# Optimization experiments

Hardware: AMD Instinct MI355X
Metric: run time of the kernel (lower is better)

The kernel has to match this reference:

```python
import jax, jax.numpy as jnp
import numpy as np

N_NODES = 20000
N_EDGES = 320000
HEADS = 4
N_REL = 40
F_IN = 768
HID = 128
N_CLS = 9


def setup_inputs() -> dict:
    key = jax.random.key(0)
    ks = jax.random.split(key, 32)
    s = 0.05
    inp = {
        'x': jax.random.normal(ks[0], (N_NODES, F_IN), jnp.float32),
        'edge_index': jax.random.randint(ks[1], (2, N_EDGES), 0, N_NODES, jnp.int64),
        'edge_type': jax.random.randint(ks[2], (N_EDGES,), 0, N_REL, jnp.int64),
        'edge_distance': jax.random.randint(ks[3], (N_EDGES,), 0, 10, jnp.int32),
        'W0': jax.random.normal(ks[4], (HEADS, F_IN, HID), jnp.float32) * s,
        'asrc0': jax.random.normal(ks[5], (HEADS, HID), jnp.float32) * s,
        'adst0': jax.random.normal(ks[6], (HEADS, HID), jnp.float32) * s,
        'aedge0': jax.random.normal(ks[7], (HEADS, 2), jnp.float32) * s,
        'b0': jnp.zeros((HID,), jnp.float32),
        'rel0': jax.random.normal(ks[8], (N_REL, 2), jnp.float32) * s,
        'Wm': jax.random.normal(ks[9], (3, HEADS, HID, HID), jnp.float32) * s,
        'asrcm': jax.random.normal(ks[10], (3, HEADS, HID), jnp.float32) * s,
        'adstm': jax.random.normal(ks[11], (3, HEADS, HID), jnp.float32) * s,
        'aedgem': jax.random.normal(ks[12], (3, HEADS, 2), jnp.float32) * s,
        'bm': jnp.zeros((3, HID), jnp.float32),
        'relm': jax.random.normal(ks[13], (3, N_REL, 2), jnp.float32) * s,
        'WL': jax.random.normal(ks[14], (HEADS, HID, N_CLS), jnp.float32) * s,
        'asrcL': jax.random.normal(ks[15], (HEADS, N_CLS), jnp.float32) * s,
        'adstL': jax.random.normal(ks[16], (HEADS, N_CLS), jnp.float32) * s,
        'aedgeL': jax.random.normal(ks[17], (HEADS, 2), jnp.float32) * s,
        'bL': jnp.zeros((N_CLS,), jnp.float32),
        'relL': jax.random.normal(ks[18], (N_REL, 2), jnp.float32) * s,
        'bn_gamma': jnp.ones((4, HID), jnp.float32),
        'bn_beta': jnp.zeros((4, HID), jnp.float32),
    }
    return inp


def _bn(x, g, b):
    # BatchNorm1d with batch statistics (training mode), eps=1e-5
    mu = x.mean(0)
    var = ((x - mu) ** 2).mean(0)
    return (x - mu) * jax.lax.rsqrt(var + 1e-5) * g + b


def _argcn_conv(x, src, dst, etype, distw, W, a_s, a_d, a_e, b, rel, n):
    # multi-head relational graph attention conv with distance decay
    h = jnp.einsum('nf,hfo->nho', x, W)                       # [N,H,O]
    es = jnp.einsum('nho,ho->nh', h, a_s)                     # [N,H]
    ed = jnp.einsum('nho,ho->nh', h, a_d)                     # [N,H]
    ee = rel[etype] @ a_e.T                                   # [E,H]
    logit = jax.nn.leaky_relu(es[src] + ed[dst] + ee, 0.2)    # [E,H]
    m = jax.ops.segment_max(logit, dst, num_segments=n)
    ex = jnp.exp(logit - m[dst])
    den = jax.ops.segment_sum(ex, dst, num_segments=n)
    alpha = ex / (den[dst] + 1e-16) * distw[:, None]          # [E,H]
    out = jax.ops.segment_sum(alpha[:, :, None] * h[src], dst, num_segments=n)  # [N,H,O]
    return out.mean(axis=1) + b


def reference(x, edge_index, edge_type, edge_distance,
              W0, asrc0, adst0, aedge0, b0, rel0,
              Wm, asrcm, adstm, aedgem, bm, relm,
              WL, asrcL, adstL, aedgeL, bL, relL,
              bn_gamma, bn_beta):
    n = x.shape[0]
    src, dst = edge_index[0], edge_index[1]
    distw = 1.0 / (1.0 + edge_distance.astype(jnp.float32))
    x = _argcn_conv(x, src, dst, edge_type, distw, W0, asrc0, adst0, aedge0, b0, rel0, n)
    for i in range(3):
        h = jax.nn.leaky_relu(_bn(x, bn_gamma[i], bn_beta[i]), 0.1)
        x = _argcn_conv(h, src, dst, edge_type, distw, Wm[i], asrcm[i], adstm[i], aedgem[i], bm[i], relm[i], n) + h
    h = jax.nn.leaky_relu(_bn(x, bn_gamma[3], bn_beta[3]), 0.1)
    x = _argcn_conv(h, src, dst, edge_type, distw, WL, asrcL, adstL, aedgeL, bL, relL, n)
    return jax.nn.leaky_relu(x, 0.1)
```

## Files before the change

### kernel.cpp

```cpp
#include <hip/hip_runtime.h>
#include <math.h>

#define NN   20000
#define NE   320000
#define NH   4
#define NREL 40
#define FIN  768
#define HIDD 128
#define NCLS 9
#define MAXDEG 128

typedef __attribute__((ext_vector_type(8))) short short8;
typedef __attribute__((ext_vector_type(4))) float f32x4;
typedef unsigned short b16;

__device__ __forceinline__ float lrelu(float v, float s) { return v > 0.f ? v : v * s; }
__device__ __forceinline__ b16 f2b(float f) {
    unsigned int u = __float_as_uint(f);
    unsigned int r = u + 0x7FFFu + ((u >> 16) & 1u);
    return (b16)(r >> 16);
}
__device__ __forceinline__ float b2f(b16 u) { return __uint_as_float(((unsigned int)u) << 16); }

__global__ void k_zero(float* p, int n) {
    int i = blockIdx.x * blockDim.x + threadIdx.x;
    if (i < n) p[i] = 0.f;
}
__global__ void k_copy_i32(int* d, const int* s, int n) {
    int i = blockIdx.x * blockDim.x + threadIdx.x;
    if (i < n) d[i] = s[i];
}

__global__ void k_count(const int* __restrict__ dst, int* __restrict__ counts) {
    int e = blockIdx.x * blockDim.x + threadIdx.x;
    if (e < NE) atomicAdd(&counts[dst[e]], 1);
}
__global__ void k_scan(const int* __restrict__ counts, int* __restrict__ rowptr) {
    __shared__ int sh[1024];
    int t = threadIdx.x;
    int base = t * 20;
    int sum = 0;
    if (t < 1000) for (int k = 0; k < 20; ++k) sum += counts[base + k];
    sh[t] = sum;
    __syncthreads();
    for (int off = 1; off < 1024; off <<= 1) {
        int v = (t >= off) ? sh[t - off] : 0;
        __syncthreads();
        sh[t] += v;
        __syncthreads();
    }
    int ex = (t == 0) ? 0 : sh[t - 1];
    if (t == 0) rowptr[0] = 0;
    if (t < 1000) {
        int run = ex;
        for (int k = 0; k < 20; ++k) {
            run += counts[base + k];
            rowptr[base + k + 1] = run;
        }
    }
}
__global__ void k_fill(const int* __restrict__ dst, int* __restrict__ cursor, int* __restrict__ eidx) {
    int e = blockIdx.x * blockDim.x + threadIdx.x;
    if (e < NE) {
        int pos = atomicAdd(&cursor[dst[e]], 1);
        eidx[pos] = e;
    }
}
__global__ void k_permute(const int* __restrict__ eidx, const int* __restrict__ src,
                          const int* __restrict__ etype, const int* __restrict__ dist,
                          int* __restrict__ srcp, int* __restrict__ etp,
                          float* __restrict__ distwp) {
    int p = blockIdx.x * blockDim.x + threadIdx.x;
    if (p >= NE) return;
    int e = eidx[p];
    srcp[p] = src[e];
    etp[p] = etype[e];
    distwp[p] = 1.f / (1.f + (float)dist[e]);
}

__global__ void k_etab(const float* __restrict__ rel0, const float* __restrict__ relm,
                       const float* __restrict__ relL, const float* __restrict__ ae0,
                       const float* __restrict__ aem, const float* __restrict__ aeL,
                       float* __restrict__ etab) {
    int id = blockIdx.x * blockDim.x + threadIdx.x;
    if (id >= 5 * NREL * NH) return;
    int tab = id / (NREL * NH);
    int rem = id % (NREL * NH);
    int t = rem >> 2, h = rem & 3;
    const float *rel, *ae;
    if (tab == 0)      { rel = rel0;                        ae = ae0; }
    else if (tab <= 3) { rel = relm + (tab - 1) * NREL * 2; ae = aem + (tab - 1) * NH * 2; }
    else               { rel = relL;                        ae = aeL; }
    etab[id] = rel[t * 2] * ae[h * 2] + rel[t * 2 + 1] * ae[h * 2 + 1];
}
__global__ void k_wsm(const float* __restrict__ Wm, const float* __restrict__ asrcm,
                      const float* __restrict__ adstm, float* __restrict__ wsm,
                      float* __restrict__ wdm) {
    int id = blockIdx.x * blockDim.x + threadIdx.x;
    if (id >= 2 * 3 * NH * HIDD) return;
    int which = id / (3 * NH * HIDD);
    int r = id % (3 * NH * HIDD);
    int ih = r / HIDD;
    int f = r % HIDD;
    const float* w = Wm + ((size_t)ih * HIDD + f) * HIDD;
    const float* a = (which ? adstm : asrcm) + ih * HIDD;
    float acc = 0.f;
    for (int o = 0; o < HIDD; ++o) acc += w[o] * a[o];
    (which ? wdm : wsm)[r] = acc;
}

__global__ void k_cast_bf16(const float* __restrict__ in, b16* __restrict__ out, int n4) {
    int i = blockIdx.x * blockDim.x + threadIdx.x;
    if (i >= n4) return;
    float4 v = ((const float4*)in)[i];
    ushort4 o;
    o.x = f2b(v.x); o.y = f2b(v.y); o.z = f2b(v.z); o.w = f2b(v.w);
    ((ushort4*)out)[i] = o;
}
__global__ void k_convB0(const float* __restrict__ W0, b16* __restrict__ B0t) {
    int id = blockIdx.x * blockDim.x + threadIdx.x;
    if (id >= 512 * FIN) return;
    int c = id / FIN, k = id % FIN;
    int h = c >> 7, o = c & 127;
    B0t[id] = f2b(W0[((size_t)h * FIN + k) * HIDD + o]);
}
__global__ void k_convBm(const float* __restrict__ Wm, b16* __restrict__ Bmt) {
    int id = blockIdx.x * blockDim.x + threadIdx.x;
    if (id >= 3 * HIDD * 512) return;
    int i = id / (HIDD * 512);
    int r = id % (HIDD * 512);
    int o = r / 512, hf = r % 512;
    Bmt[id] = f2b(Wm[(size_t)i * 512 * HIDD + (size_t)hf * HIDD + o]);
}
__global__ void k_convBL(const float* __restrict__ WL, b16* __restrict__ WLt) {
    int id = blockIdx.x * blockDim.x + threadIdx.x;
    if (id >= 48 * HIDD) return;
    int cf = id / HIDD, k = id % HIDD;
    float v = 0.f;
    if (cf < 36) {
        int h = cf / 9, c = cf % 9;
        v = WL[((size_t)h * HIDD + k) * NCLS + c];
    }
    WLt[id] = f2b(v);
}

__global__ __launch_bounds__(256) void k_mfma_gemm(
    const b16* __restrict__ A, const b16* __restrict__ Bt, int M, int K, int N,
    float scl, b16* __restrict__ Cb, float* __restrict__ Cf,
    const float* __restrict__ bias, const float* __restrict__ resid,
    const float* __restrict__ asv, const float* __restrict__ adv,
    float* __restrict__ esp, float* __restrict__ edp) {
    __shared__ b16 As[128][40];
    __shared__ b16 Bs[128][40];
    __shared__ float sc_es[2][128];
    __shared__ float sc_ed[2][128];
    int tid = threadIdx.x;
    int lane = tid & 63, wave = tid >> 6;
    int wm = wave >> 1, wn = wave & 1;
    int l16 = lane & 15, quad = lane >> 4;
    int row0 = blockIdx.x * 128, col0 = blockIdx.y * 128;

    int c0 = tid, c1 = tid + 256;
    int ar0 = c0 >> 2, as0 = (c0 & 3) << 3;
    int ar1 = c1 >> 2, as1 = (c1 & 3) << 3;
    bool va0 = (row0 + ar0) < M, va1 = (row0 + ar1) < M;
    const b16* Ap0 = A + (size_t)(row0 + ar0) * K + as0;
    const b16* Ap1 = A + (size_t)(row0 + ar1) * K + as1;
    const b16* Bp0 = Bt + (size_t)(col0 + ar0) * K + as0;
    const b16* Bp1 = Bt + (size_t)(col0 + ar1) * K + as1;

    f32x4 acc[4][4];
#pragma unroll
    for (int i = 0; i < 4; ++i)
#pragma unroll
        for (int j = 0; j < 4; ++j) acc[i][j] = (f32x4){0.f, 0.f, 0.f, 0.f};
    short8 zz = {0, 0, 0, 0, 0, 0, 0, 0};

    for (int kt = 0; kt < K; kt += 32) {
        short8 a0 = va0 ? *(const short8*)(Ap0 + kt) : zz;
        short8 a1 = va1 ? *(const short8*)(Ap1 + kt) : zz;
        short8 b0 = *(const short8*)(Bp0 + kt);
        short8 b1 = *(const short8*)(Bp1 + kt);
        __syncthreads();
        *(short8*)&As[ar0][as0] = a0;
        *(short8*)&As[ar1][as1] = a1;
        *(short8*)&Bs[ar0][as0] = b0;
        *(short8*)&Bs[ar1][as1] = b1;
        __syncthreads();
        short8 bf[4];
#pragma unroll
        for (int ni = 0; ni < 4; ++ni)
            bf[ni] = *(const short8*)&Bs[wn * 64 + ni * 16 + l16][quad * 8];
#pragma unroll
        for (int mi = 0; mi < 4; ++mi) {
            short8 af = *(const short8*)&As[wm * 64 + mi * 16 + l16][quad * 8];
#pragma unroll
            for (int ni = 0; ni < 4; ++ni)
                acc[mi][ni] = __builtin_amdgcn_mfma_f32_16x16x32_bf16(af, bf[ni], acc[mi][ni], 0, 0, 0);
        }
    }
    if (Cb) {
#pragma unroll
        for (int mi = 0; mi < 4; ++mi) {
            int rb = row0 + wm * 64 + mi * 16 + quad * 4;
#pragma unroll
            for (int ni = 0; ni < 4; ++ni) {
                int c = col0 + wn * 64 + ni * 16 + l16;
#pragma unroll
                for (int r = 0; r < 4; ++r) {
                    int row = rb + r;
                    if (row < M) Cb[(size_t)row * N + c] = f2b(acc[mi][ni][r]);
                }
            }
        }
    } else {
#pragma unroll
        for (int mi = 0; mi < 4; ++mi) {
            int rb = row0 + wm * 64 + mi * 16 + quad * 4;
#pragma unroll
            for (int ni = 0; ni < 4; ++ni) {
                int c = col0 + wn * 64 + ni * 16 + l16;
#pragma unroll
                for (int r = 0; r < 4; ++r) {
                    int row = rb + r;
                    if (row < M) {
                        float v = acc[mi][ni][r] * scl + bias[c] + resid[(size_t)row * N + c];
                        Cf[(size_t)row * N + c] = v;
                    }
                }
            }
        }
    }
    if (esp) {
        int h = blockIdx.y;
        float as_c[4], ad_c[4];
#pragma unroll
        for (int ni = 0; ni < 4; ++ni) {
            int c = wn * 64 + ni * 16 + l16;
            as_c[ni] = asv[h * 128 + c];
            ad_c[ni] = adv[h * 128 + c];
        }
#pragma unroll
        for (int mi = 0; mi < 4; ++mi) {
#pragma unroll
            for (int r = 0; r < 4; ++r) {
                float pes = 0.f, ped = 0.f;
#pragma unroll
                for (int ni = 0; ni < 4; ++ni) {
                    float v = acc[mi][ni][r];
                    pes += v * as_c[ni];
                    ped += v * ad_c[ni];
                }
#pragma unroll
                for (int m = 1; m < 16; m <<= 1) {
                    pes += __shfl_xor(pes, m, 64);
                    ped += __shfl_xor(ped, m, 64);
                }
                if (l16 == 0) {
                    int rl = wm * 64 + mi * 16 + quad * 4 + r;
                    sc_es[wn][rl] = pes;
                    sc_ed[wn][rl] = ped;
                }
            }
        }
        __syncthreads();
        if (tid < 128) {
            int row = row0 + tid;
            if (row < M) {
                esp[row * 4 + h] = sc_es[0][tid] + sc_es[1][tid];
                edp[row * 4 + h] = sc_ed[0][tid] + sc_ed[1][tid];
            }
        }
    }
}

__global__ __launch_bounds__(256) void k_gemmL_mfma(
    const b16* __restrict__ hbb, const b16* __restrict__ WLt, float* __restrict__ hL) {
    int tid = threadIdx.x;
    int lane = tid & 63, wave = tid >> 6;
    int l16 = lane & 15, quad = lane >> 4;
    int base = blockIdx.x * 64 + wave * 16;
    int na = base + l16;
    f32x4 acc[3];
#pragma unroll
    for (int ct = 0; ct < 3; ++ct) acc[ct] = (f32x4){0.f, 0.f, 0.f, 0.f};
    short8 zz = {0, 0, 0, 0, 0, 0, 0, 0};
#pragma unroll
    for (int k0 = 0; k0 < 128; k0 += 32) {
        short8 af = (na < NN) ? *(const short8*)(hbb + (size_t)na * HIDD + k0 + quad * 8) : zz;
#pragma unroll
        for (int ct = 0; ct < 3; ++ct) {
            short8 bf = *(const short8*)(WLt + (size_t)(ct * 16 + l16) * HIDD + k0 + quad * 8);
            acc[ct] = __builtin_amdgcn_mfma_f32_16x16x32_bf16(af, bf, acc[ct], 0, 0, 0);
        }
    }
#pragma unroll
    for (int ct = 0; ct < 3; ++ct) {
        int col = ct * 16 + l16;
        if (col < 36) {
#pragma unroll
            for (int r = 0; r < 4; ++r) {
                int row = base + quad * 4 + r;
                if (row < NN) hL[(size_t)row * 36 + col] = acc[ct][r];
            }
        }
    }
}

__global__ void k_scoresL(const float* __restrict__ hL, const float* __restrict__ aS,
                          const float* __restrict__ aD, float* __restrict__ es,
                          float* __restrict__ ed) {
    int n = blockIdx.x * blockDim.x + threadIdx.x;
    if (n >= NN) return;
    for (int h = 0; h < NH; ++h) {
        float s = 0.f, d = 0.f;
        for (int c = 0; c < NCLS; ++c) {
            float v = hL[(size_t)n * 36 + h * 9 + c];
            s += v * aS[h * 9 + c];
            d += v * aD[h * 9 + c];
        }
        es[n * 4 + h] = s;
        ed[n * 4 + h] = d;
    }
}

__global__ __launch_bounds__(64) void k_agg0_f(
    const int* __restrict__ rowptr, const int* __restrict__ srcp,
    const int* __restrict__ etpp, const float* __restrict__ distwp,
    const float* __restrict__ es, const float* __restrict__ ed,
    const float* __restrict__ etab, const b16* __restrict__ h0b,
    const float* __restrict__ b0, float* __restrict__ xout) {
    __shared__ float4 exw[MAXDEG];
    int n = blockIdx.x, t = threadIdx.x;
    int p0 = rowptr[n], p1 = rowptr[n + 1];
    int deg = p1 - p0;
    float4 edn = ((const float4*)ed)[n];
    float d0 = 0.f, d1 = 0.f, d2 = 0.f, d3 = 0.f;
    for (int p = p0 + t; p < p1; p += 64) {
        int s = srcp[p], ty = etpp[p];
        float w = distwp[p];
        float4 a = ((const float4*)es)[s];
        float4 c = ((const float4*)etab)[ty];
        float e0 = __expf(lrelu(a.x + edn.x + c.x, 0.2f));
        float e1 = __expf(lrelu(a.y + edn.y + c.y, 0.2f));
        float e2 = __expf(lrelu(a.z + edn.z + c.z, 0.2f));
        float e3 = __expf(lrelu(a.w + edn.w + c.w, 0.2f));
        d0 += e0; d1 += e1; d2 += e2; d3 += e3;
        int ix = p - p0;
        if (ix < MAXDEG) exw[ix] = make_float4(e0 * w, e1 * w, e2 * w, e3 * w);
    }
#pragma unroll
    for (int off = 32; off > 0; off >>= 1) {
        d0 += __shfl_down(d0, off, 64);
        d1 += __shfl_down(d1, off, 64);
        d2 += __shfl_down(d2, off, 64);
        d3 += __shfl_down(d3, off, 64);
    }
    d0 = __shfl(d0, 0, 64); d1 = __shfl(d1, 0, 64);
    d2 = __shfl(d2, 0, 64); d3 = __shfl(d3, 0, 64);
    float r0 = 1.f / (d0 + 1e-16f), r1 = 1.f / (d1 + 1e-16f);
    float r2 = 1.f / (d2 + 1e-16f), r3 = 1.f / (d3 + 1e-16f);
    __syncthreads();
    float acc0 = 0.f, acc1 = 0.f;
    int tt = t * 2;
    if (deg <= MAXDEG) {
        int p = p0;
        for (; p + 4 <= p1; p += 4) {
            int ib = p - p0;
            int ss[4]; float4 ee[4];
#pragma unroll
            for (int j = 0; j < 4; ++j) { ss[j] = srcp[p + j]; ee[j] = exw[ib + j]; }
#pragma unroll
            for (int j = 0; j < 4; ++j) {
                const b16* hr = h0b + (size_t)ss[j] * 512;
                ushort2 u0 = *(const ushort2*)(hr + tt);
                ushort2 u1 = *(const ushort2*)(hr + 128 + tt);
                ushort2 u2 = *(const ushort2*)(hr + 256 + tt);
                ushort2 u3 = *(const ushort2*)(hr + 384 + tt);
                float c0 = ee[j].x * r0, c1 = ee[j].y * r1;
                float c2 = ee[j].z * r2, c3 = ee[j].w * r3;
                acc0 += c0 * b2f(u0.x) + c1 * b2f(u1.x) + c2 * b2f(u2.x) + c3 * b2f(u3.x);
                acc1 += c0 * b2f(u0.y) + c1 * b2f(u1.y) + c2 * b2f(u2.y) + c3 * b2f(u3.y);
            }
        }
        for (; p < p1; ++p) {
            int s = srcp[p];
            float4 e = exw[p - p0];
            const b16* hr = h0b + (size_t)s * 512;
            ushort2 u0 = *(const ushort2*)(hr + tt);
            ushort2 u1 = *(const ushort2*)(hr + 128 + tt);
            ushort2 u2 = *(const ushort2*)(hr + 256 + tt);
            ushort2 u3 = *(const ushort2*)(hr + 384 + tt);
            float c0 = e.x * r0, c1 = e.y * r1, c2 = e.z * r2, c3 = e.w * r3;
            acc0 += c0 * b2f(u0.x) + c1 * b2f(u1.x) + c2 * b2f(u2.x) + c3 * b2f(u3.x);
            acc1 += c0 * b2f(u0.y) + c1 * b2f(u1.y) + c2 * b2f(u2.y) + c3 * b2f(u3.y);
        }
    } else {
        for (int p = p0; p < p1; ++p) {
            int s = srcp[p];
            int ix = p - p0;
            float4 e;
            if (ix < MAXDEG) e = exw[ix];
            else {
                int ty = etpp[p];
                float w = distwp[p];
                float4 a = ((const float4*)es)[s];
                float4 c = ((const float4*)etab)[ty];
                e.x = __expf(lrelu(a.x + edn.x + c.x, 0.2f)) * w;
                e.y = __expf(lrelu(a.y + edn.y + c.y, 0.2f)) * w;
                e.z = __expf(lrelu(a.z + edn.z + c.z, 0.2f)) * w;
                e.w = __expf(lrelu(a.w + edn.w + c.w, 0.2f)) * w;
            }
            const b16* hr = h0b + (size_t)s * 512;
            ushort2 u0 = *(const ushort2*)(hr + tt);
            ushort2 u1 = *(const ushort2*)(hr + 128 + tt);
            ushort2 u2 = *(const ushort2*)(hr + 256 + tt);
            ushort2 u3 = *(const ushort2*)(hr + 384 + tt);
            float c0 = e.x * r0, c1 = e.y * r1, c2 = e.z * r2, c3 = e.w * r3;
            acc0 += c0 * b2f(u0.x) + c1 * b2f(u1.x) + c2 * b2f(u2.x) + c3 * b2f(u3.x);
            acc1 += c0 * b2f(u0.y) + c1 * b2f(u1.y) + c2 * b2f(u2.y) + c3 * b2f(u3.y);
        }
    }
    xout[(size_t)n * HIDD + tt] = 0.25f * acc0 + b0[tt];
    xout[(size_t)n * HIDD + tt + 1] = 0.25f * acc1 + b0[tt + 1];
}
__global__ __launch_bounds__(64) void k_aggmid_f(
    const int* __restrict__ rowptr, const int* __restrict__ srcp,
    const int* __restrict__ etpp, const float* __restrict__ distwp,
    const float* __restrict__ es, const float* __restrict__ ed,
    const float* __restrict__ etab, const b16* __restrict__ hbb,
    b16* __restrict__ aggb) {
    __shared__ float4 exw[MAXDEG];
    int n = blockIdx.x, t = threadIdx.x;
    int p0 = rowptr[n], p1 = rowptr[n + 1];
    int deg = p1 - p0;
    float4 edn = ((const float4*)ed)[n];
    float d0 = 0.f, d1 = 0.f, d2 = 0.f, d3 = 0.f;
    for (int p = p0 + t; p < p1; p += 64) {
        int s = srcp[p], ty = etpp[p];
        float w = distwp[p];
        float4 a = ((const float4*)es)[s];
        float4 c = ((const float4*)etab)[ty];
        float e0 = __expf(lrelu(a.x + edn.x + c.x, 0.2f));
        float e1 = __expf(lrelu(a.y + edn.y + c.y, 0.2f));
        float e2 = __expf(lrelu(a.z + edn.z + c.z, 0.2f));
        float e3 = __expf(lrelu(a.w + edn.w + c.w, 0.2f));
        d0 += e0; d1 += e1; d2 += e2; d3 += e3;
        int ix = p - p0;
        if (ix < MAXDEG) exw[ix] = make_float4(e0 * w, e1 * w, e2 * w, e3 * w);
    }
#pragma unroll
    for (int off = 32; off > 0; off >>= 1) {
        d0 += __shfl_down(d0, off, 64);
        d1 += __shfl_down(d1, off, 64);
        d2 += __shfl_down(d2, off, 64);
        d3 += __shfl_down(d3, off, 64);
    }
    d0 = __shfl(d0, 0, 64); d1 = __shfl(d1, 0, 64);
    d2 = __shfl(d2, 0, 64); d3 = __shfl(d3, 0, 64);
    float r0 = 1.f / (d0 + 1e-16f), r1 = 1.f / (d1 + 1e-16f);
    float r2 = 1.f / (d2 + 1e-16f), r3 = 1.f / (d3 + 1e-16f);
    __syncthreads();
    float a00 = 0.f, a01 = 0.f, a10 = 0.f, a11 = 0.f;
    float a20 = 0.f, a21 = 0.f, a30 = 0.f, a31 = 0.f;
    int tt = t * 2;
    if (deg <= MAXDEG) {
        int p = p0;
        for (; p + 4 <= p1; p += 4) {
            int ib = p - p0;
            int ss[4]; float4 ee[4];
#pragma unroll
            for (int j = 0; j < 4; ++j) { ss[j] = srcp[p + j]; ee[j] = exw[ib + j]; }
#pragma unroll
            for (int j = 0; j < 4; ++j) {
                ushort2 u = *(const ushort2*)(hbb + (size_t)ss[j] * HIDD + tt);
                float f0 = b2f(u.x), f1 = b2f(u.y);
                float c0 = ee[j].x * r0, c1 = ee[j].y * r1;
                float c2 = ee[j].z * r2, c3 = ee[j].w * r3;
                a00 += c0 * f0; a01 += c0 * f1;
                a10 += c1 * f0; a11 += c1 * f1;
                a20 += c2 * f0; a21 += c2 * f1;
                a30 += c3 * f0; a31 += c3 * f1;
            }
        }
        for (; p < p1; ++p) {
            int s = srcp[p];
            float4 e = exw[p - p0];
            ushort2 u = *(const ushort2*)(hbb + (size_t)s * HIDD + tt);
            float f0 = b2f(u.x), f1 = b2f(u.y);
            float c0 = e.x * r0, c1 = e.y * r1, c2 = e.z * r2, c3 = e.w * r3;
            a00 += c0 * f0; a01 += c0 * f1;
            a10 += c1 * f0; a11 += c1 * f1;
            a20 += c2 * f0; a21 += c2 * f1;
            a30 += c3 * f0; a31 += c3 * f1;
        }
    } else {
        for (int p = p0; p < p1; ++p) {
            int s = srcp[p];
            int ix = p - p0;
            float4 e;
            if (ix < MAXDEG) e = exw[ix];
            else {
                int ty = etpp[p];
                float w = distwp[p];
                float4 a = ((const float4*)es)[s];
                float4 c = ((const float4*)etab)[ty];
                e.x = __expf(lrelu(a.x + edn.x + c.x, 0.2f)) * w;
                e.y = __expf(lrelu(a.y + edn.y + c.y, 0.2f)) * w;
                e.z = __expf(lrelu(a.z + edn.z + c.z, 0.2f)) * w;
                e.w = __expf(lrelu(a.w + edn.w + c.w, 0.2f)) * w;
            }
            ushort2 u = *(const ushort2*)(hbb + (size_t)s * HIDD + tt);
            float f0 = b2f(u.x), f1 = b2f(u.y);
            float c0 = e.x * r0, c1 = e.y * r1, c2 = e.z * r2, c3 = e.w * r3;
            a00 += c0 * f0; a01 += c0 * f1;
            a10 += c1 * f0; a11 += c1 * f1;
            a20 += c2 * f0; a21 += c2 * f1;
            a30 += c3 * f0; a31 += c3 * f1;
        }
    }
    b16* o = aggb + (size_t)n * 512;
    ushort2 w0; w0.x = f2b(a00); w0.y = f2b(a01); *(ushort2*)(o + tt) = w0;
    ushort2 w1; w1.x = f2b(a10); w1.y = f2b(a11); *(ushort2*)(o + 128 + tt) = w1;
    ushort2 w2; w2.x = f2b(a20); w2.y = f2b(a21); *(ushort2*)(o + 256 + tt) = w2;
    ushort2 w3; w3.x = f2b(a30); w3.y = f2b(a31); *(ushort2*)(o + 384 + tt) = w3;
}
__global__ __launch_bounds__(64) void k_aggL_f(
    const int* __restrict__ rowptr, const int* __restrict__ srcp,
    const int* __restrict__ etpp, const float* __restrict__ distwp,
    const float* __restrict__ es, const float* __restrict__ ed,
    const float* __restrict__ etab, const float* __restrict__ hL,
    const float* __restrict__ bL, float* __restrict__ out) {
    __shared__ float4 exw[MAXDEG];
    __shared__ float sh[40];
    int n = blockIdx.x, t = threadIdx.x;
    int p0 = rowptr[n], p1 = rowptr[n + 1];
    float4 edn = ((const float4*)ed)[n];
    float d0 = 0.f, d1 = 0.f, d2 = 0.f, d3 = 0.f;
    for (int p = p0 + t; p < p1; p += 64) {
        int s = srcp[p], ty = etpp[p];
        float w = distwp[p];
        float4 a = ((const float4*)es)[s];
        float4 c = ((const float4*)etab)[ty];
        float e0 = __expf(lrelu(a.x + edn.x + c.x, 0.2f));
        float e1 = __expf(lrelu(a.y + edn.y + c.y, 0.2f));
        float e2 = __expf(lrelu(a.z + edn.z + c.z, 0.2f));
        float e3 = __expf(lrelu(a.w + edn.w + c.w, 0.2f));
        d0 += e0; d1 += e1; d2 += e2; d3 += e3;
        int ix = p - p0;
        if (ix < MAXDEG) exw[ix] = make_float4(e0 * w, e1 * w, e2 * w, e3 * w);
    }
#pragma unroll
    for (int off = 32; off > 0; off >>= 1) {
        d0 += __shfl_down(d0, off, 64);
        d1 += __shfl_down(d1, off, 64);
        d2 += __shfl_down(d2, off, 64);
        d3 += __shfl_down(d3, off, 64);
    }
    d0 = __shfl(d0, 0, 64); d1 = __shfl(d1, 0, 64);
    d2 = __shfl(d2, 0, 64); d3 = __shfl(d3, 0, 64);
    __syncthreads();
    if (t < 36) {
        int hh = t / 9;
        float rv = (hh == 0) ? 1.f / (d0 + 1e-16f)
                 : (hh == 1) ? 1.f / (d1 + 1e-16f)
                 : (hh == 2) ? 1.f / (d2 + 1e-16f)
                             : 1.f / (d3 + 1e-16f);
        float acc = 0.f;
        for (int p = p0; p < p1; ++p) {
            int s = srcp[p];
            int ix = p - p0;
            float av;
            if (ix < MAXDEG) {
                float4 e = exw[ix];
                av = (hh == 0) ? e.x : (hh == 1) ? e.y : (hh == 2) ? e.z : e.w;
            } else {
                int ty = etpp[p];
                float w = distwp[p];
                float a4 = ((const float4*)es)[s].x;
                float4 a = ((const float4*)es)[s];
                float4 c = ((const float4*)etab)[ty];
                float lv = (hh == 0) ? a.x + edn.x + c.x
                         : (hh == 1) ? a.y + edn.y + c.y
                         : (hh == 2) ? a.z + edn.z + c.z
                                     : a.w + edn.w + c.w;
                av = __expf(lrelu(lv, 0.2f)) * w;
                (void)a4;
            }
            acc += av * rv * hL[(size_t)s * 36 + t];
        }
        sh[t] = acc;
    }
    __syncthreads();
    if (t < 9) {
        float v = 0.25f * (sh[t] + sh[t + 9] + sh[t + 18] + sh[t + 27]) + bL[t];
        out[(size_t)n * 9 + t] = lrelu(v, 0.1f);
    }
}

__global__ __launch_bounds__(128) void k_bnstats(const float* __restrict__ x, float* __restrict__ partial) {
    int f = threadIdx.x;
    float s = 0.f, q = 0.f;
    for (int r = blockIdx.x; r < NN; r += gridDim.x) {
        float v = x[(size_t)r * HIDD + f];
        s += v;
        q += v * v;
    }
    partial[blockIdx.x * 256 + f] = s;
    partial[blockIdx.x * 256 + 128 + f] = q;
}
__global__ void k_bnfinal(const float* __restrict__ partial, const float* __restrict__ gamma,
                          const float* __restrict__ beta, float* __restrict__ scale,
                          float* __restrict__ shift) {
    int f = threadIdx.x;
    float s = 0.f, q = 0.f;
    for (int j = 0; j < 200; ++j) {
        s += partial[j * 256 + f];
        q += partial[j * 256 + 128 + f];
    }
    float m = s * (1.f / NN);
    float v = q * (1.f / NN) - m * m;
    float sc = gamma[f] * rsqrtf(v + 1e-5f);
    scale[f] = sc;
    shift[f] = beta[f] - m * sc;
}
__global__ __launch_bounds__(64) void k_bnaps(
    const float* __restrict__ x, const float* __restrict__ scale,
    const float* __restrict__ shift, const float* __restrict__ Ws,
    const float* __restrict__ Wd, float* __restrict__ hb, b16* __restrict__ hbb,
    float* __restrict__ es, float* __restrict__ ed) {
    int n = blockIdx.x, t = threadIdx.x;
    float2 xv = ((const float2*)(x + (size_t)n * HIDD))[t];
    float2 sc = ((const float2*)scale)[t];
    float2 sh = ((const float2*)shift)[t];
    float y0 = lrelu(xv.x * sc.x + sh.x, 0.1f);
    float y1 = lrelu(xv.y * sc.y + sh.y, 0.1f);
    ((float2*)(hb + (size_t)n * HIDD))[t] = make_float2(y0, y1);
    ushort2 ub; ub.x = f2b(y0); ub.y = f2b(y1);
    ((ushort2*)(hbb + (size_t)n * HIDD))[t] = ub;
    if (Ws) {
        float pe[4], pd[4];
        int tt = t * 2;
#pragma unroll
        for (int h = 0; h < 4; ++h) {
            pe[h] = y0 * Ws[h * 128 + tt] + y1 * Ws[h * 128 + tt + 1];
            pd[h] = y0 * Wd[h * 128 + tt] + y1 * Wd[h * 128 + tt + 1];
        }
#pragma unroll
        for (int off = 32; off > 0; off >>= 1) {
#pragma unroll
            for (int h = 0; h < 4; ++h) {
                pe[h] += __shfl_down(pe[h], off, 64);
                pd[h] += __shfl_down(pd[h], off, 64);
            }
        }
        if (t == 0) {
#pragma unroll
            for (int h = 0; h < 4; ++h) {
                es[n * 4 + h] = pe[h];
                ed[n * 4 + h] = pd[h];
            }
        }
    }
}

extern "C" void kernel_launch(void* const* d_in, const int* in_sizes, int n_in,
                              void* d_out, int out_size, void* d_ws, size_t ws_size,
                              hipStream_t stream) {
    const float* x = (const float*)d_in[0];
    const int* ei = (const int*)d_in[1];
    const int* src = ei;
    const int* dst = ei + NE;
    const int* etype = (const int*)d_in[2];
    const int* edist = (const int*)d_in[3];
    const float* W0 = (const float*)d_in[4];
    const float* asrc0 = (const float*)d_in[5];
    const float* adst0 = (const float*)d_in[6];
    const float* aedge0 = (const float*)d_in[7];
    const float* b0 = (const float*)d_in[8];
    const float* rel0 = (const float*)d_in[9];
    const float* Wm = (const float*)d_in[10];
    const float* asrcm = (const float*)d_in[11];
    const float* adstm = (const float*)d_in[12];
    const float* aedgem = (const float*)d_in[13];
    const float* bm = (const float*)d_in[14];
    const float* relm = (const float*)d_in[15];
    const float* WL = (const float*)d_in[16];
    const float* asrcL = (const float*)d_in[17];
    const float* adstL = (const float*)d_in[18];
    const float* aedgeL = (const float*)d_in[19];
    const float* bL = (const float*)d_in[20];
    const float* relL = (const float*)d_in[21];
    const float* bng = (const float*)d_in[22];
    const float* bnb = (const float*)d_in[23];
    float* out = (float*)d_out;

    char* w = (char*)d_ws;
    size_t off = 0;
    auto alloc = [&](size_t bytes) -> char* {
        char* p = w + off;
        off = (off + bytes + 255) & ~(size_t)255;
        return p;
    };
    char* ws0 = alloc((size_t)NN * FIN * 2);
    b16* xb = (b16*)ws0;
    float* xbuf = (float*)ws0;
    float* hb = (float*)(ws0 + 10240000);
    float* hL = (float*)(ws0 + 20480000);
    b16* h0b = (b16*)alloc((size_t)NN * 512 * 2);
    b16* B0t = (b16*)alloc((size_t)512 * FIN * 2);
    b16* Bmt = (b16*)alloc((size_t)3 * HIDD * 512 * 2);
    b16* WLt = (b16*)alloc((size_t)48 * HIDD * 2);
    b16* hbb = (b16*)alloc((size_t)NN * HIDD * 2);
    float* es = (float*)alloc((size_t)NN * 4 * 4);
    float* ed = (float*)alloc((size_t)NN * 4 * 4);
    int* srcp = (int*)alloc((size_t)NE * 4);
    int* etpp = (int*)alloc((size_t)NE * 4);
    float* distwp = (float*)alloc((size_t)NE * 4);
    int* eidx = (int*)alloc((size_t)NE * 4);
    float* bnpart = (float*)alloc((size_t)200 * 256 * 4);
    float* scale = (float*)alloc(128 * 4);
    float* shift = (float*)alloc(128 * 4);
    float* wsmb = (float*)alloc(1536 * 4);
    float* wdmb = (float*)alloc(1536 * 4);
    float* etab = (float*)alloc(800 * 4);
    int* counts = (int*)alloc((size_t)NN * 4);
    int* rowptr = (int*)alloc((size_t)(NN + 1) * 4);
    int* cursor = (int*)alloc((size_t)NN * 4);

    const int B256 = 256;
    int gNE = (NE + 255) / 256;
    int gNN = (NN + 255) / 256;

    k_zero<<<gNN, B256, 0, stream>>>((float*)counts, NN);
    k_count<<<gNE, B256, 0, stream>>>(dst, counts);
    k_scan<<<1, 1024, 0, stream>>>(counts, rowptr);
    k_copy_i32<<<gNN, B256, 0, stream>>>(cursor, rowptr, NN);
    k_fill<<<gNE, B256, 0, stream>>>(dst, cursor, eidx);
    k_permute<<<gNE, B256, 0, stream>>>(eidx, src, etype, edist, srcp, etpp, distwp);

    k_etab<<<4, B256, 0, stream>>>(rel0, relm, relL, aedge0, aedgem, aedgeL, etab);
    k_wsm<<<12, B256, 0, stream>>>(Wm, asrcm, adstm, wsmb, wdmb);
    k_cast_bf16<<<(NN * FIN / 4 + 255) / 256, B256, 0, stream>>>(x, xb, NN * FIN / 4);
    k_convB0<<<(512 * FIN + 255) / 256, B256, 0, stream>>>(W0, B0t);
    k_convBm<<<(3 * HIDD * 512 + 255) / 256, B256, 0, stream>>>(Wm, Bmt);
    k_convBL<<<(48 * HIDD + 255) / 256, B256, 0, stream>>>(WL, WLt);

    int mblk = (NN + 127) / 128;

    {
        dim3 g(mblk, 4);
        k_mfma_gemm<<<g, 256, 0, stream>>>(xb, B0t, NN, FIN, 512, 1.f, h0b, nullptr,
                                           nullptr, nullptr, asrc0, adst0, es, ed);
        k_agg0_f<<<NN, 64, 0, stream>>>(rowptr, srcp, etpp, distwp, es, ed, etab + 0,
                                        h0b, b0, xbuf);
    }

    for (int i = 0; i < 3; ++i) {
        k_bnstats<<<200, 128, 0, stream>>>(xbuf, bnpart);
        k_bnfinal<<<1, 128, 0, stream>>>(bnpart, bng + i * 128, bnb + i * 128, scale, shift);
        k_bnaps<<<NN, 64, 0, stream>>>(xbuf, scale, shift, wsmb + i * 512, wdmb + i * 512,
                                       hb, hbb, es, ed);
        k_aggmid_f<<<NN, 64, 0, stream>>>(rowptr, srcp, etpp, distwp, es, ed,
                                          etab + (1 + i) * 160, hbb, h0b);
        dim3 g(mblk, 1);
        k_mfma_gemm<<<g, 256, 0, stream>>>(h0b, Bmt + (size_t)i * HIDD * 512, NN, 512, HIDD,
                                           0.25f, nullptr, xbuf, bm + i * 128, hb,
                                           nullptr, nullptr, nullptr, nullptr);
    }

    {
        k_bnstats<<<200, 128, 0, stream>>>(xbuf, bnpart);
        k_bnfinal<<<1, 128, 0, stream>>>(bnpart, bng + 3 * 128, bnb + 3 * 128, scale, shift);
        k_bnaps<<<NN, 64, 0, stream>>>(xbuf, scale, shift, nullptr, nullptr, hb, hbb, es, ed);
        k_gemmL_mfma<<<(NN + 63) / 64, 256, 0, stream>>>(hbb, WLt, hL);
        k_scoresL<<<gNN, B256, 0, stream>>>(hL, asrcL, adstL, es, ed);
        k_aggL_f<<<NN, 64, 0, stream>>>(rowptr, srcp, etpp, distwp, es, ed, etab + 4 * 160,
                                        hL, bL, out);
    }
}
```

Measured before the change: 663.1 us.

## Fuse setup kernels, BN stats into GEMM epilogue, and scores into final GEMM

Several small preprocessing kernels are merged into two launches (tables and casts). BatchNorm statistics are accumulated by atomics inside the mid-layer GEMM epilogue, and normalization finalization moves into the apply kernel, which drops the separate stats and final kernels. The final-layer attention scores are computed in the GEMM epilogue, and the mid GEMM uses 64-row tiles for more blocks. Aggregation kernels are reorganized so each thread handles 4 contiguous channels over half the heads. Atomic float sums add nondeterminism, and the single-pass variance formula is kept.

```diff
diff --git a/kernel.cpp b/kernel.cpp
--- a/kernel.cpp
+++ b/kernel.cpp
@@ -22,9 +22,10 @@
 }
 __device__ __forceinline__ float b2f(b16 u) { return __uint_as_float(((unsigned int)u) << 16); }
 
-__global__ void k_zero(float* p, int n) {
+__global__ void k_init(int* __restrict__ counts, float* __restrict__ sums) {
     int i = blockIdx.x * blockDim.x + threadIdx.x;
-    if (i < n) p[i] = 0.f;
+    if (i < NN) counts[i] = 0;
+    if (i < 1024) sums[i] = 0.f;
 }
 __global__ void k_copy_i32(int* d, const int* s, int n) {
     int i = blockIdx.x * blockDim.x + threadIdx.x;
@@ -78,77 +79,82 @@
     distwp[p] = 1.f / (1.f + (float)dist[e]);
 }
 
-__global__ void k_etab(const float* __restrict__ rel0, const float* __restrict__ relm,
-                       const float* __restrict__ relL, const float* __restrict__ ae0,
-                       const float* __restrict__ aem, const float* __restrict__ aeL,
-                       float* __restrict__ etab) {
+__global__ void k_tables(const float* __restrict__ rel0, const float* __restrict__ relm,
+                         const float* __restrict__ relL, const float* __restrict__ ae0,
+                         const float* __restrict__ aem, const float* __restrict__ aeL,
+                         const float* __restrict__ Wm, const float* __restrict__ asrcm,
+                         const float* __restrict__ adstm, const float* __restrict__ WL,
+                         const float* __restrict__ asrcL, const float* __restrict__ adstL,
+                         float* __restrict__ etab, float* __restrict__ wsm,
+                         float* __restrict__ wdm, b16* __restrict__ WLt,
+                         float* __restrict__ aS48, float* __restrict__ aD48) {
     int id = blockIdx.x * blockDim.x + threadIdx.x;
-    if (id >= 5 * NREL * NH) return;
-    int tab = id / (NREL * NH);
-    int rem = id % (NREL * NH);
-    int t = rem >> 2, h = rem & 3;
-    const float *rel, *ae;
-    if (tab == 0)      { rel = rel0;                        ae = ae0; }
-    else if (tab <= 3) { rel = relm + (tab - 1) * NREL * 2; ae = aem + (tab - 1) * NH * 2; }
-    else               { rel = relL;                        ae = aeL; }
-    etab[id] = rel[t * 2] * ae[h * 2] + rel[t * 2 + 1] * ae[h * 2 + 1];
-}
-__global__ void k_wsm(const float* __restrict__ Wm, const float* __restrict__ asrcm,
-                      const float* __restrict__ adstm, float* __restrict__ wsm,
-                      float* __restrict__ wdm) {
+    if (id < 800) {
+        int tab = id / (NREL * NH);
+        int rem = id % (NREL * NH);
+        int t = rem >> 2, h = rem & 3;
+        const float *rel, *ae;
+        if (tab == 0)      { rel = rel0;                        ae = ae0; }
+        else if (tab <= 3) { rel = relm + (tab - 1) * NREL * 2; ae = aem + (tab - 1) * NH * 2; }
+        else               { rel = relL;                        ae = aeL; }
+        etab[id] = rel[t * 2] * ae[h * 2] + rel[t * 2 + 1] * ae[h * 2 + 1];
+    } else if (id < 3872) {
+        int id2 = id - 800;
+        int which = id2 / 1536;
+        int r = id2 % 1536;
+        int ih = r / HIDD;
+        int f = r % HIDD;
+        const float* w = Wm + ((size_t)ih * HIDD + f) * HIDD;
+        const float* a = (which ? adstm : asrcm) + ih * HIDD;
+        float acc = 0.f;
+        for (int o = 0; o < HIDD; ++o) acc += w[o] * a[o];
+        (which ? wdm : wsm)[r] = acc;
+    } else if (id < 10016) {
+        int id3 = id - 3872;
+        int cf = id3 / HIDD, k = id3 % HIDD;
+        float v = 0.f;
+        if (cf < 36) {
+            int h = cf / 9, c = cf % 9;
+            v = WL[((size_t)h * HIDD + k) * NCLS + c];
+        }
+        WLt[id3] = f2b(v);
+    } else if (id < 10112) {
+        int id4 = id - 10016;
+        int c = id4 % 48;
+        float v = (c < 36) ? ((id4 < 48) ? asrcL[c] : adstL[c]) : 0.f;
+        if (id4 < 48) aS48[c] = v; else aD48[c] = v;
+    }
+}
+
+#define XCAST4   3840000
+#define B0_END   4233216
+#define BM_END   4429824
+__global__ void k_casts(const float* __restrict__ x, const float* __restrict__ W0,
+                        const float* __restrict__ Wm, b16* __restrict__ xb,
+                        b16* __restrict__ B0t, b16* __restrict__ Bmt) {
     int id = blockIdx.x * blockDim.x + threadIdx.x;
-    if (id >= 2 * 3 * NH * HIDD) return;
-    int which = id / (3 * NH * HIDD);
-    int r = id % (3 * NH * HIDD);
-    int ih = r / HIDD;
-    int f = r % HIDD;
-    const float* w = Wm + ((size_t)ih * HIDD + f) * HIDD;
-    const float* a = (which ? adstm : asrcm) + ih * HIDD;
-    float acc = 0.f;
-    for (int o = 0; o < HIDD; ++o) acc += w[o] * a[o];
-    (which ? wdm : wsm)[r] = acc;
-}
-
-__global__ void k_cast_bf16(const float* __restrict__ in, b16* __restrict__ out, int n4) {
-    int i = blockIdx.x * blockDim.x + threadIdx.x;
-    if (i >= n4) return;
-    float4 v = ((const float4*)in)[i];
-    ushort4 o;
-    o.x = f2b(v.x); o.y = f2b(v.y); o.z = f2b(v.z); o.w = f2b(v.w);
-    ((ushort4*)out)[i] = o;
-}
-__global__ void k_convB0(const float* __restrict__ W0, b16* __restrict__ B0t) {
-    int id = blockIdx.x * blockDim.x + threadIdx.x;
-    if (id >= 512 * FIN) return;
-    int c = id / FIN, k = id % FIN;
-    int h = c >> 7, o = c & 127;
-    B0t[id] = f2b(W0[((size_t)h * FIN + k) * HIDD + o]);
-}
-__global__ void k_convBm(const float* __restrict__ Wm, b16* __restrict__ Bmt) {
-    int id = blockIdx.x * blockDim.x + threadIdx.x;
-    if (id >= 3 * HIDD * 512) return;
-    int i = id / (HIDD * 512);
-    int r = id % (HIDD * 512);
-    int o = r / 512, hf = r % 512;
-    Bmt[id] = f2b(Wm[(size_t)i * 512 * HIDD + (size_t)hf * HIDD + o]);
-}
-__global__ void k_convBL(const float* __restrict__ WL, b16* __restrict__ WLt) {
-    int id = blockIdx.x * blockDim.x + threadIdx.x;
-    if (id >= 48 * HIDD) return;
-    int cf = id / HIDD, k = id % HIDD;
-    float v = 0.f;
-    if (cf < 36) {
-        int h = cf / 9, c = cf % 9;
-        v = WL[((size_t)h * HIDD + k) * NCLS + c];
-    }
-    WLt[id] = f2b(v);
+    if (id < XCAST4) {
+        float4 v = ((const float4*)x)[id];
+        ushort4 o;
+        o.x = f2b(v.x); o.y = f2b(v.y); o.z = f2b(v.z); o.w = f2b(v.w);
+        ((ushort4*)xb)[id] = o;
+    } else if (id < B0_END) {
+        int i = id - XCAST4;
+        int c = i / FIN, k = i % FIN;
+        int h = c >> 7, o = c & 127;
+        B0t[i] = f2b(W0[((size_t)h * FIN + k) * HIDD + o]);
+    } else if (id < BM_END) {
+        int i = id - B0_END;
+        int l = i / (HIDD * 512);
+        int r = i % (HIDD * 512);
+        int o = r / 512, hf = r % 512;
+        Bmt[i] = f2b(Wm[(size_t)l * 512 * HIDD + (size_t)hf * HIDD + o]);
+    }
 }
 
 __global__ __launch_bounds__(256) void k_mfma_gemm(
     const b16* __restrict__ A, const b16* __restrict__ Bt, int M, int K, int N,
-    float scl, b16* __restrict__ Cb, float* __restrict__ Cf,
-    const float* __restrict__ bias, const float* __restrict__ resid,
-    const float* __restrict__ asv, const float* __restrict__ adv,
+    b16* __restrict__ Cb, const float* __restrict__ asv, const float* __restrict__ adv,
     float* __restrict__ esp, float* __restrict__ edp) {
     __shared__ b16 As[128][40];
     __shared__ b16 Bs[128][40];
@@ -199,39 +205,20 @@
                 acc[mi][ni] = __builtin_amdgcn_mfma_f32_16x16x32_bf16(af, bf[ni], acc[mi][ni], 0, 0, 0);
         }
     }
-    if (Cb) {
-#pragma unroll
-        for (int mi = 0; mi < 4; ++mi) {
-            int rb = row0 + wm * 64 + mi * 16 + quad * 4;
-#pragma unroll
-            for (int ni = 0; ni < 4; ++ni) {
-                int c = col0 + wn * 64 + ni * 16 + l16;
-#pragma unroll
-                for (int r = 0; r < 4; ++r) {
-                    int row = rb + r;
-                    if (row < M) Cb[(size_t)row * N + c] = f2b(acc[mi][ni][r]);
-                }
-            }
-        }
-    } else {
-#pragma unroll
-        for (int mi = 0; mi < 4; ++mi) {
-            int rb = row0 + wm * 64 + mi * 16 + quad * 4;
-#pragma unroll
-            for (int ni = 0; ni < 4; ++ni) {
-                int c = col0 + wn * 64 + ni * 16 + l16;
-#pragma unroll
-                for (int r = 0; r < 4; ++r) {
-                    int row = rb + r;
-                    if (row < M) {
-                        float v = acc[mi][ni][r] * scl + bias[c] + resid[(size_t)row * N + c];
-                        Cf[(size_t)row * N + c] = v;
-                    }
-                }
-            }
-        }
-    }
-    if (esp) {
+#pragma unroll
+    for (int mi = 0; mi < 4; ++mi) {
+        int rb = row0 + wm * 64 + mi * 16 + quad * 4;
+#pragma unroll
+        for (int ni = 0; ni < 4; ++ni) {
+            int c = col0 + wn * 64 + ni * 16 + l16;
+#pragma unroll
+            for (int r = 0; r < 4; ++r) {
+                int row = rb + r;
+                if (row < M) Cb[(size_t)row * N + c] = f2b(acc[mi][ni][r]);
+            }
+        }
+    }
+    {
         int h = blockIdx.y;
         float as_c[4], ad_c[4];
 #pragma unroll
@@ -274,8 +261,104 @@
     }
 }
 
+__global__ __launch_bounds__(128) void k_gemm_mid(
+    const b16* __restrict__ A, const b16* __restrict__ Bt, float* __restrict__ Cf,
+    const float* __restrict__ bias, const float* __restrict__ resid,
+    float* __restrict__ sums) {
+    __shared__ b16 As[64][40];
+    __shared__ b16 Bs[128][40];
+    int tid = threadIdx.x;
+    int lane = tid & 63, wave = tid >> 6;
+    int l16 = lane & 15, quad = lane >> 4;
+    int row0 = blockIdx.x * 64;
+    const int K = 512;
+
+    int ar[2], asg[2]; bool av[2];
+    const b16* Ap[2];
+#pragma unroll
+    for (int j = 0; j < 2; ++j) {
+        int c = tid + j * 128;
+        ar[j] = c >> 2; asg[j] = (c & 3) << 3;
+        int grow = row0 + ar[j];
+        av[j] = grow < NN;
+        Ap[j] = A + (size_t)(av[j] ? grow : 0) * K + asg[j];
+    }
+    int br[4], bsg[4];
+    const b16* Bp[4];
+#pragma unroll
+    for (int j = 0; j < 4; ++j) {
+        int c = tid + j * 128;
+        br[j] = c >> 2; bsg[j] = (c & 3) << 3;
+        Bp[j] = Bt + (size_t)br[j] * K + bsg[j];
+    }
+
+    f32x4 acc[4][4];
+#pragma unroll
+    for (int i = 0; i < 4; ++i)
+#pragma unroll
+        for (int j = 0; j < 4; ++j) acc[i][j] = (f32x4){0.f, 0.f, 0.f, 0.f};
+    short8 zz = {0, 0, 0, 0, 0, 0, 0, 0};
+
+    for (int kt = 0; kt < K; kt += 32) {
+        short8 a[2], b[4];
+#pragma unroll
+        for (int j = 0; j < 2; ++j) a[j] = av[j] ? *(const short8*)(Ap[j] + kt) : zz;
+#pragma unroll
+        for (int j = 0; j < 4; ++j) b[j] = *(const short8*)(Bp[j] + kt);
+        __syncthreads();
+#pragma unroll
+        for (int j = 0; j < 2; ++j) *(short8*)&As[ar[j]][asg[j]] = a[j];
+#pragma unroll
+        for (int j = 0; j < 4; ++j) *(short8*)&Bs[br[j]][bsg[j]] = b[j];
+        __syncthreads();
+        short8 bf[4];
+#pragma unroll
+        for (int ni = 0; ni < 4; ++ni)
+            bf[ni] = *(const short8*)&Bs[wave * 64 + ni * 16 + l16][quad * 8];
+#pragma unroll
+        for (int mi = 0; mi < 4; ++mi) {
+            short8 af = *(const short8*)&As[mi * 16 + l16][quad * 8];
+#pragma unroll
+            for (int ni = 0; ni < 4; ++ni)
+                acc[mi][ni] = __builtin_amdgcn_mfma_f32_16x16x32_bf16(af, bf[ni], acc[mi][ni], 0, 0, 0);
+        }
+    }
+    float sp[4] = {0.f, 0.f, 0.f, 0.f}, qp[4] = {0.f, 0.f, 0.f, 0.f};
+#pragma unroll
+    for (int mi = 0; mi < 4; ++mi) {
+        int rb = row0 + mi * 16 + quad * 4;
+#pragma unroll
+        for (int ni = 0; ni < 4; ++ni) {
+            int c = wave * 64 + ni * 16 + l16;
+#pragma unroll
+            for (int r = 0; r < 4; ++r) {
+                int row = rb + r;
+                if (row < NN) {
+                    float v = acc[mi][ni][r] * 0.25f + bias[c] + resid[(size_t)row * HIDD + c];
+                    Cf[(size_t)row * HIDD + c] = v;
+                    sp[ni] += v;
+                    qp[ni] += v * v;
+                }
+            }
+        }
+    }
+#pragma unroll
+    for (int ni = 0; ni < 4; ++ni) {
+        float s = sp[ni], q = qp[ni];
+        s += __shfl_xor(s, 16, 64); s += __shfl_xor(s, 32, 64);
+        q += __shfl_xor(q, 16, 64); q += __shfl_xor(q, 32, 64);
+        if (quad == 0) {
+            int c = wave * 64 + ni * 16 + l16;
+            atomicAdd(&sums[c], s);
+            atomicAdd(&sums[128 + c], q);
+        }
+    }
+}
+
 __global__ __launch_bounds__(256) void k_gemmL_mfma(
-    const b16* __restrict__ hbb, const b16* __restrict__ WLt, float* __restrict__ hL) {
+    const b16* __restrict__ hbb, const b16* __restrict__ WLt, float* __restrict__ hL,
+    const float* __restrict__ aS48, const float* __restrict__ aD48,
+    float* __restrict__ es, float* __restrict__ ed) {
     int tid = threadIdx.x;
     int lane = tid & 63, wave = tid >> 6;
     int l16 = lane & 15, quad = lane >> 4;
@@ -305,22 +388,45 @@
             }
         }
     }
-}
-
-__global__ void k_scoresL(const float* __restrict__ hL, const float* __restrict__ aS,
-                          const float* __restrict__ aD, float* __restrict__ es,
-                          float* __restrict__ ed) {
-    int n = blockIdx.x * blockDim.x + threadIdx.x;
-    if (n >= NN) return;
-    for (int h = 0; h < NH; ++h) {
-        float s = 0.f, d = 0.f;
-        for (int c = 0; c < NCLS; ++c) {
-            float v = hL[(size_t)n * 36 + h * 9 + c];
-            s += v * aS[h * 9 + c];
-            d += v * aD[h * 9 + c];
-        }
-        es[n * 4 + h] = s;
-        ed[n * 4 + h] = d;
+    float asv[3], adv[3]; int hh[3];
+#pragma unroll
+    for (int ct = 0; ct < 3; ++ct) {
+        int col = ct * 16 + l16;
+        asv[ct] = aS48[col];
+        adv[ct] = aD48[col];
+        hh[ct] = (col < 36) ? (col / 9) : 0;
+    }
+#pragma unroll
+    for (int r = 0; r < 4; ++r) {
+        float pes[4] = {0.f, 0.f, 0.f, 0.f}, ped[4] = {0.f, 0.f, 0.f, 0.f};
+#pragma unroll
+        for (int ct = 0; ct < 3; ++ct) {
+            float vs = acc[ct][r] * asv[ct];
+            float vd = acc[ct][r] * adv[ct];
+#pragma unroll
+            for (int h = 0; h < 4; ++h) {
+                pes[h] += (hh[ct] == h) ? vs : 0.f;
+                ped[h] += (hh[ct] == h) ? vd : 0.f;
+            }
+        }
+#pragma unroll
+        for (int m = 1; m < 16; m <<= 1) {
+#pragma unroll
+            for (int h = 0; h < 4; ++h) {
+                pes[h] += __shfl_xor(pes[h], m, 64);
+                ped[h] += __shfl_xor(ped[h], m, 64);
+            }
+        }
+        if (l16 == 0) {
+            int row = base + quad * 4 + r;
+            if (row < NN) {
+#pragma unroll
+                for (int h = 0; h < 4; ++h) {
+                    es[row * 4 + h] = pes[h];
+                    ed[row * 4 + h] = ped[h];
+                }
+            }
+        }
     }
 }
 
@@ -331,6 +437,7 @@
     const float* __restrict__ etab, const b16* __restrict__ h0b,
     const float* __restrict__ b0, float* __restrict__ xout) {
     __shared__ float4 exw[MAXDEG];
+    __shared__ float comb[32][4];
     int n = blockIdx.x, t = threadIdx.x;
     int p0 = rowptr[n], p1 = rowptr[n + 1];
     int deg = p1 - p0;
@@ -361,39 +468,42 @@
     float r0 = 1.f / (d0 + 1e-16f), r1 = 1.f / (d1 + 1e-16f);
     float r2 = 1.f / (d2 + 1e-16f), r3 = 1.f / (d3 + 1e-16f);
     __syncthreads();
-    float acc0 = 0.f, acc1 = 0.f;
-    int tt = t * 2;
+    int half = t >> 5, q = t & 31;
+    int cq = q * 4;
+    float ra = half ? r2 : r0, rb = half ? r3 : r1;
+    int sega = half * 256;
+    float acc[4] = {0.f, 0.f, 0.f, 0.f};
     if (deg <= MAXDEG) {
         int p = p0;
         for (; p + 4 <= p1; p += 4) {
-            int ib = p - p0;
             int ss[4]; float4 ee[4];
 #pragma unroll
-            for (int j = 0; j < 4; ++j) { ss[j] = srcp[p + j]; ee[j] = exw[ib + j]; }
+            for (int j = 0; j < 4; ++j) { ss[j] = srcp[p + j]; ee[j] = exw[p - p0 + j]; }
 #pragma unroll
             for (int j = 0; j < 4; ++j) {
-                const b16* hr = h0b + (size_t)ss[j] * 512;
-                ushort2 u0 = *(const ushort2*)(hr + tt);
-                ushort2 u1 = *(const ushort2*)(hr + 128 + tt);
-                ushort2 u2 = *(const ushort2*)(hr + 256 + tt);
-                ushort2 u3 = *(const ushort2*)(hr + 384 + tt);
-                float c0 = ee[j].x * r0, c1 = ee[j].y * r1;
-                float c2 = ee[j].z * r2, c3 = ee[j].w * r3;
-                acc0 += c0 * b2f(u0.x) + c1 * b2f(u1.x) + c2 * b2f(u2.x) + c3 * b2f(u3.x);
-                acc1 += c0 * b2f(u0.y) + c1 * b2f(u1.y) + c2 * b2f(u2.y) + c3 * b2f(u3.y);
+                float ca = (half ? ee[j].z : ee[j].x) * ra;
+                float cb = (half ? ee[j].w : ee[j].y) * rb;
+                const b16* hr = h0b + (size_t)ss[j] * 512 + sega + cq;
+                ushort4 ua = *(const ushort4*)(hr);
+                ushort4 ub = *(const ushort4*)(hr + 128);
+                acc[0] += ca * b2f(ua.x) + cb * b2f(ub.x);
+                acc[1] += ca * b2f(ua.y) + cb * b2f(ub.y);
+                acc[2] += ca * b2f(ua.z) + cb * b2f(ub.z);
+                acc[3] += ca * b2f(ua.w) + cb * b2f(ub.w);
             }
         }
         for (; p < p1; ++p) {
             int s = srcp[p];
             float4 e = exw[p - p0];
-            const b16* hr = h0b + (size_t)s * 512;
-            ushort2 u0 = *(const ushort2*)(hr + tt);
-            ushort2 u1 = *(const ushort2*)(hr + 128 + tt);
-            ushort2 u2 = *(const ushort2*)(hr + 256 + tt);
-            ushort2 u3 = *(const ushort2*)(hr + 384 + tt);
-            float c0 = e.x * r0, c1 = e.y * r1, c2 = e.z * r2, c3 = e.w * r3;
-            acc0 += c0 * b2f(u0.x) + c1 * b2f(u1.x) + c2 * b2f(u2.x) + c3 * b2f(u3.x);
-            acc1 += c0 * b2f(u0.y) + c1 * b2f(u1.y) + c2 * b2f(u2.y) + c3 * b2f(u3.y);
+            float ca = (half ? e.z : e.x) * ra;
+            float cb = (half ? e.w : e.y) * rb;
+            const b16* hr = h0b + (size_t)s * 512 + sega + cq;
+            ushort4 ua = *(const ushort4*)(hr);
+            ushort4 ub = *(const ushort4*)(hr + 128);
+            acc[0] += ca * b2f(ua.x) + cb * b2f(ub.x);
+            acc[1] += ca * b2f(ua.y) + cb * b2f(ub.y);
+            acc[2] += ca * b2f(ua.z) + cb * b2f(ub.z);
+            acc[3] += ca * b2f(ua.w) + cb * b2f(ub.w);
         }
     } else {
         for (int p = p0; p < p1; ++p) {
@@ -411,18 +521,30 @@
                 e.z = __expf(lrelu(a.z + edn.z + c.z, 0.2f)) * w;
                 e.w = __expf(lrelu(a.w + edn.w + c.w, 0.2f)) * w;
             }
-            const b16* hr = h0b + (size_t)s * 512;
-            ushort2 u0 = *(const ushort2*)(hr + tt);
-            ushort2 u1 = *(const ushort2*)(hr + 128 + tt);
-            ushort2 u2 = *(const ushort2*)(hr + 256 + tt);
-            ushort2 u3 = *(const ushort2*)(hr + 384 + tt);
-            float c0 = e.x * r0, c1 = e.y * r1, c2 = e.z * r2, c3 = e.w * r3;
-            acc0 += c0 * b2f(u0.x) + c1 * b2f(u1.x) + c2 * b2f(u2.x) + c3 * b2f(u3.x);
-            acc1 += c0 * b2f(u0.y) + c1 * b2f(u1.y) + c2 * b2f(u2.y) + c3 * b2f(u3.y);
-        }
-    }
-    xout[(size_t)n * HIDD + tt] = 0.25f * acc0 + b0[tt];
-    xout[(size_t)n * HIDD + tt + 1] = 0.25f * acc1 + b0[tt + 1];
+            float ca = (half ? e.z : e.x) * ra;
+            float cb = (half ? e.w : e.y) * rb;
+            const b16* hr = h0b + (size_t)s * 512 + sega + cq;
+            ushort4 ua = *(const ushort4*)(hr);
+            ushort4 ub = *(const ushort4*)(hr + 128);
+            acc[0] += ca * b2f(ua.x) + cb * b2f(ub.x);
+            acc[1] += ca * b2f(ua.y) + cb * b2f(ub.y);
+            acc[2] += ca * b2f(ua.z) + cb * b2f(ub.z);
+            acc[3] += ca * b2f(ua.w) + cb * b2f(ub.w);
+        }
+    }
+    if (half == 1) {
+        comb[q][0] = acc[0]; comb[q][1] = acc[1];
+        comb[q][2] = acc[2]; comb[q][3] = acc[3];
+    }
+    __syncthreads();
+    if (half == 0) {
+        float4 o;
+        o.x = 0.25f * (acc[0] + comb[q][0]) + b0[cq];
+        o.y = 0.25f * (acc[1] + comb[q][1]) + b0[cq + 1];
+        o.z = 0.25f * (acc[2] + comb[q][2]) + b0[cq + 2];
+        o.w = 0.25f * (acc[3] + comb[q][3]) + b0[cq + 3];
+        *(float4*)(xout + (size_t)n * HIDD + cq) = o;
+    }
 }
 __global__ __launch_bounds__(64) void k_aggmid_f(
     const int* __restrict__ rowptr, const int* __restrict__ srcp,
@@ -431,6 +553,7 @@
     const float* __restrict__ etab, const b16* __restrict__ hbb,
     b16* __restrict__ aggb) {
     __shared__ float4 exw[MAXDEG];
+    __shared__ float comb[32][16];
     int n = blockIdx.x, t = threadIdx.x;
     int p0 = rowptr[n], p1 = rowptr[n + 1];
     int deg = p1 - p0;
@@ -461,41 +584,33 @@
     float r0 = 1.f / (d0 + 1e-16f), r1 = 1.f / (d1 + 1e-16f);
     float r2 = 1.f / (d2 + 1e-16f), r3 = 1.f / (d3 + 1e-16f);
     __syncthreads();
-    float a00 = 0.f, a01 = 0.f, a10 = 0.f, a11 = 0.f;
-    float a20 = 0.f, a21 = 0.f, a30 = 0.f, a31 = 0.f;
-    int tt = t * 2;
+    int half = t >> 5, q = t & 31;
+    int cq = q * 4;
+    float acc[4][4];
+#pragma unroll
+    for (int h = 0; h < 4; ++h)
+#pragma unroll
+        for (int j = 0; j < 4; ++j) acc[h][j] = 0.f;
+    auto doE = [&](int s, float4 e) {
+        float c0 = e.x * r0, c1 = e.y * r1, c2 = e.z * r2, c3 = e.w * r3;
+        ushort4 u = *(const ushort4*)(hbb + (size_t)s * HIDD + cq);
+        float f0 = b2f(u.x), f1 = b2f(u.y), f2 = b2f(u.z), f3 = b2f(u.w);
+        acc[0][0] += c0 * f0; acc[0][1] += c0 * f1; acc[0][2] += c0 * f2; acc[0][3] += c0 * f3;
+        acc[1][0] += c1 * f0; acc[1][1] += c1 * f1; acc[1][2] += c1 * f2; acc[1][3] += c1 * f3;
+        acc[2][0] += c2 * f0; acc[2][1] += c2 * f1; acc[2][2] += c2 * f2; acc[2][3] += c2 * f3;
+        acc[3][0] += c3 * f0; acc[3][1] += c3 * f1; acc[3][2] += c3 * f2; acc[3][3] += c3 * f3;
+    };
     if (deg <= MAXDEG) {
-        int p = p0;
-        for (; p + 4 <= p1; p += 4) {
-            int ib = p - p0;
-            int ss[4]; float4 ee[4];
-#pragma unroll
-            for (int j = 0; j < 4; ++j) { ss[j] = srcp[p + j]; ee[j] = exw[ib + j]; }
-#pragma unroll
-            for (int j = 0; j < 4; ++j) {
-                ushort2 u = *(const ushort2*)(hbb + (size_t)ss[j] * HIDD + tt);
-                float f0 = b2f(u.x), f1 = b2f(u.y);
-                float c0 = ee[j].x * r0, c1 = ee[j].y * r1;
-                float c2 = ee[j].z * r2, c3 = ee[j].w * r3;
-                a00 += c0 * f0; a01 += c0 * f1;
-                a10 += c1 * f0; a11 += c1 * f1;
-                a20 += c2 * f0; a21 += c2 * f1;
-                a30 += c3 * f0; a31 += c3 * f1;
-            }
-        }
-        for (; p < p1; ++p) {
-            int s = srcp[p];
-            float4 e = exw[p - p0];
-            ushort2 u = *(const ushort2*)(hbb + (size_t)s * HIDD + tt);
-            float f0 = b2f(u.x), f1 = b2f(u.y);
-            float c0 = e.x * r0, c1 = e.y * r1, c2 = e.z * r2, c3 = e.w * r3;
-            a00 += c0 * f0; a01 += c0 * f1;
-            a10 += c1 * f0; a11 += c1 * f1;
-            a20 += c2 * f0; a21 += c2 * f1;
-            a30 += c3 * f0; a31 += c3 * f1;
-        }
+        int p = p0 + half;
+        for (; p + 2 < p1; p += 4) {
+            int s0 = srcp[p], s1 = srcp[p + 2];
+            float4 e0 = exw[p - p0], e1 = exw[p + 2 - p0];
+            doE(s0, e0);
+            doE(s1, e1);
+        }
+        for (; p < p1; p += 2) doE(srcp[p], exw[p - p0]);
     } else {
-        for (int p = p0; p < p1; ++p) {
+        for (int p = p0 + half; p < p1; p += 2) {
             int s = srcp[p];
             int ix = p - p0;
             float4 e;
@@ -510,20 +625,28 @@
                 e.z = __expf(lrelu(a.z + edn.z + c.z, 0.2f)) * w;
                 e.w = __expf(lrelu(a.w + edn.w + c.w, 0.2f)) * w;
             }
-            ushort2 u = *(const ushort2*)(hbb + (size_t)s * HIDD + tt);
-            float f0 = b2f(u.x), f1 = b2f(u.y);
-            float c0 = e.x * r0, c1 = e.y * r1, c2 = e.z * r2, c3 = e.w * r3;
-            a00 += c0 * f0; a01 += c0 * f1;
-            a10 += c1 * f0; a11 += c1 * f1;
-            a20 += c2 * f0; a21 += c2 * f1;
-            a30 += c3 * f0; a31 += c3 * f1;
-        }
-    }
-    b16* o = aggb + (size_t)n * 512;
-    ushort2 w0; w0.x = f2b(a00); w0.y = f2b(a01); *(ushort2*)(o + tt) = w0;
-    ushort2 w1; w1.x = f2b(a10); w1.y = f2b(a11); *(ushort2*)(o + 128 + tt) = w1;
-    ushort2 w2; w2.x = f2b(a20); w2.y = f2b(a21); *(ushort2*)(o + 256 + tt) = w2;
-    ushort2 w3; w3.x = f2b(a30); w3.y = f2b(a31); *(ushort2*)(o + 384 + tt) = w3;
+            doE(s, e);
+        }
+    }
+    if (half == 1) {
+#pragma unroll
+        for (int h = 0; h < 4; ++h)
+#pragma unroll
+            for (int j = 0; j < 4; ++j) comb[q][h * 4 + j] = acc[h][j];
+    }
+    __syncthreads();
+    if (half == 0) {
+        b16* o = aggb + (size_t)n * 512;
+#pragma unroll
+        for (int h = 0; h < 4; ++h) {
+            ushort4 w4;
+            w4.x = f2b(acc[h][0] + comb[q][h * 4 + 0]);
+            w4.y = f2b(acc[h][1] + comb[q][h * 4 + 1]);
+            w4.z = f2b(acc[h][2] + comb[q][h * 4 + 2]);
+            w4.w = f2b(acc[h][3] + comb[q][h * 4 + 3]);
+            *(ushort4*)(o + h * 128 + cq) = w4;
+        }
+    }
 }
 __global__ __launch_bounds__(64) void k_aggL_f(
     const int* __restrict__ rowptr, const int* __restrict__ srcp,
@@ -535,6 +658,7 @@
     __shared__ float sh[40];
     int n = blockIdx.x, t = threadIdx.x;
     int p0 = rowptr[n], p1 = rowptr[n + 1];
+    int deg = p1 - p0;
     float4 edn = ((const float4*)ed)[n];
     float d0 = 0.f, d1 = 0.f, d2 = 0.f, d3 = 0.f;
     for (int p = p0 + t; p < p1; p += 64) {
@@ -567,29 +691,50 @@
                  : (hh == 2) ? 1.f / (d2 + 1e-16f)
                              : 1.f / (d3 + 1e-16f);
         float acc = 0.f;
-        for (int p = p0; p < p1; ++p) {
-            int s = srcp[p];
-            int ix = p - p0;
-            float av;
-            if (ix < MAXDEG) {
-                float4 e = exw[ix];
-                av = (hh == 0) ? e.x : (hh == 1) ? e.y : (hh == 2) ? e.z : e.w;
-            } else {
-                int ty = etpp[p];
-                float w = distwp[p];
-                float a4 = ((const float4*)es)[s].x;
-                float4 a = ((const float4*)es)[s];
-                float4 c = ((const float4*)etab)[ty];
-                float lv = (hh == 0) ? a.x + edn.x + c.x
-                         : (hh == 1) ? a.y + edn.y + c.y
-                         : (hh == 2) ? a.z + edn.z + c.z
-                                     : a.w + edn.w + c.w;
-                av = __expf(lrelu(lv, 0.2f)) * w;
-                (void)a4;
-            }
-            acc += av * rv * hL[(size_t)s * 36 + t];
-        }
-        sh[t] = acc;
+        if (deg <= MAXDEG) {
+            int p = p0;
+            for (; p + 4 <= p1; p += 4) {
+                int ss[4]; float aw[4];
+#pragma unroll
+                for (int j = 0; j < 4; ++j) {
+                    ss[j] = srcp[p + j];
+                    float4 e = exw[p - p0 + j];
+                    aw[j] = (hh == 0) ? e.x : (hh == 1) ? e.y : (hh == 2) ? e.z : e.w;
+                }
+                float g[4];
+#pragma unroll
+                for (int j = 0; j < 4; ++j) g[j] = hL[(size_t)ss[j] * 36 + t];
+#pragma unroll
+                for (int j = 0; j < 4; ++j) acc += aw[j] * g[j];
+            }
+            for (; p < p1; ++p) {
+                float4 e = exw[p - p0];
+                float av = (hh == 0) ? e.x : (hh == 1) ? e.y : (hh == 2) ? e.z : e.w;
+                acc += av * hL[(size_t)srcp[p] * 36 + t];
+            }
+        } else {
+            for (int p = p0; p < p1; ++p) {
+                int s = srcp[p];
+                int ix = p - p0;
+                float av;
+                if (ix < MAXDEG) {
+                    float4 e = exw[ix];
+                    av = (hh == 0) ? e.x : (hh == 1) ? e.y : (hh == 2) ? e.z : e.w;
+                } else {
+                    int ty = etpp[p];
+                    float w = distwp[p];
+                    float4 a = ((const float4*)es)[s];
+                    float4 c = ((const float4*)etab)[ty];
+                    float lv = (hh == 0) ? a.x + edn.x + c.x
+                             : (hh == 1) ? a.y + edn.y + c.y
+                             : (hh == 2) ? a.z + edn.z + c.z
+                                         : a.w + edn.w + c.w;
+                    av = __expf(lrelu(lv, 0.2f)) * w;
+                }
+                acc += av * hL[(size_t)s * 36 + t];
+            }
+        }
+        sh[t] = acc * rv;
     }
     __syncthreads();
     if (t < 9) {
@@ -598,53 +743,45 @@
     }
 }
 
-__global__ __launch_bounds__(128) void k_bnstats(const float* __restrict__ x, float* __restrict__ partial) {
+__global__ __launch_bounds__(128) void k_bnstats_at(const float* __restrict__ x,
+                                                    float* __restrict__ sums) {
     int f = threadIdx.x;
     float s = 0.f, q = 0.f;
-    for (int r = blockIdx.x; r < NN; r += gridDim.x) {
+    for (int r = blockIdx.x; r < NN; r += 200) {
         float v = x[(size_t)r * HIDD + f];
         s += v;
         q += v * v;
     }
-    partial[blockIdx.x * 256 + f] = s;
-    partial[blockIdx.x * 256 + 128 + f] = q;
-}
-__global__ void k_bnfinal(const float* __restrict__ partial, const float* __restrict__ gamma,
-                          const float* __restrict__ beta, float* __restrict__ scale,
-                          float* __restrict__ shift) {
-    int f = threadIdx.x;
-    float s = 0.f, q = 0.f;
-    for (int j = 0; j < 200; ++j) {
-        s += partial[j * 256 + f];
-        q += partial[j * 256 + 128 + f];
-    }
-    float m = s * (1.f / NN);
-    float v = q * (1.f / NN) - m * m;
-    float sc = gamma[f] * rsqrtf(v + 1e-5f);
-    scale[f] = sc;
-    shift[f] = beta[f] - m * sc;
+    atomicAdd(&sums[f], s);
+    atomicAdd(&sums[128 + f], q);
 }
 __global__ __launch_bounds__(64) void k_bnaps(
-    const float* __restrict__ x, const float* __restrict__ scale,
-    const float* __restrict__ shift, const float* __restrict__ Ws,
-    const float* __restrict__ Wd, float* __restrict__ hb, b16* __restrict__ hbb,
+    const float* __restrict__ x, const float* __restrict__ sums,
+    const float* __restrict__ gamma, const float* __restrict__ beta,
+    const float* __restrict__ Ws, const float* __restrict__ Wd,
+    float* __restrict__ hb, b16* __restrict__ hbb,
     float* __restrict__ es, float* __restrict__ ed) {
     int n = blockIdx.x, t = threadIdx.x;
+    int c0 = t * 2;
+    float s0 = sums[c0], s1 = sums[c0 + 1];
+    float q0 = sums[128 + c0], q1 = sums[128 + c0 + 1];
+    float m0 = s0 * (1.f / NN), m1 = s1 * (1.f / NN);
+    float v0 = q0 * (1.f / NN) - m0 * m0, v1 = q1 * (1.f / NN) - m1 * m1;
+    float sc0 = gamma[c0] * rsqrtf(v0 + 1e-5f);
+    float sc1 = gamma[c0 + 1] * rsqrtf(v1 + 1e-5f);
+    float sh0 = beta[c0] - m0 * sc0, sh1 = beta[c0 + 1] - m1 * sc1;
     float2 xv = ((const float2*)(x + (size_t)n * HIDD))[t];
-    float2 sc = ((const float2*)scale)[t];
-    float2 sh = ((const float2*)shift)[t];
-    float y0 = lrelu(xv.x * sc.x + sh.x, 0.1f);
-    float y1 = lrelu(xv.y * sc.y + sh.y, 0.1f);
+    float y0 = lrelu(xv.x * sc0 + sh0, 0.1f);
+    float y1 = lrelu(xv.y * sc1 + sh1, 0.1f);
     ((float2*)(hb + (size_t)n * HIDD))[t] = make_float2(y0, y1);
     ushort2 ub; ub.x = f2b(y0); ub.y = f2b(y1);
     ((ushort2*)(hbb + (size_t)n * HIDD))[t] = ub;
     if (Ws) {
         float pe[4], pd[4];
-        int tt = t * 2;
 #pragma unroll
         for (int h = 0; h < 4; ++h) {
-            pe[h] = y0 * Ws[h * 128 + tt] + y1 * Ws[h * 128 + tt + 1];
-            pd[h] = y0 * Wd[h * 128 + tt] + y1 * Wd[h * 128 + tt + 1];
+            pe[h] = y0 * Ws[h * 128 + c0] + y1 * Ws[h * 128 + c0 + 1];
+            pd[h] = y0 * Wd[h * 128 + c0] + y1 * Wd[h * 128 + c0 + 1];
         }
 #pragma unroll
         for (int off = 32; off > 0; off >>= 1) {
@@ -718,12 +855,12 @@
     int* etpp = (int*)alloc((size_t)NE * 4);
     float* distwp = (float*)alloc((size_t)NE * 4);
     int* eidx = (int*)alloc((size_t)NE * 4);
-    float* bnpart = (float*)alloc((size_t)200 * 256 * 4);
-    float* scale = (float*)alloc(128 * 4);
-    float* shift = (float*)alloc(128 * 4);
+    float* sums = (float*)alloc(1024 * 4);
     float* wsmb = (float*)alloc(1536 * 4);
     float* wdmb = (float*)alloc(1536 * 4);
     float* etab = (float*)alloc(800 * 4);
+    float* aS48 = (float*)alloc(48 * 4);
+    float* aD48 = (float*)alloc(48 * 4);
     int* counts = (int*)alloc((size_t)NN * 4);
     int* rowptr = (int*)alloc((size_t)(NN + 1) * 4);
     int* cursor = (int*)alloc((size_t)NN * 4);
@@ -732,49 +869,42 @@
     int gNE = (NE + 255) / 256;
     int gNN = (NN + 255) / 256;
 
-    k_zero<<<gNN, B256, 0, stream>>>((float*)counts, NN);
+    k_init<<<gNN, B256, 0, stream>>>(counts, sums);
     k_count<<<gNE, B256, 0, stream>>>(dst, counts);
     k_scan<<<1, 1024, 0, stream>>>(counts, rowptr);
     k_copy_i32<<<gNN, B256, 0, stream>>>(cursor, rowptr, NN);
     k_fill<<<gNE, B256, 0, stream>>>(dst, cursor, eidx);
     k_permute<<<gNE, B256, 0, stream>>>(eidx, src, etype, edist, srcp, etpp, distwp);
 
-    k_etab<<<4, B256, 0, stream>>>(rel0, relm, relL, aedge0, aedgem, aedgeL, etab);
-    k_wsm<<<12, B256, 0, stream>>>(Wm, asrcm, adstm, wsmb, wdmb);
-    k_cast_bf16<<<(NN * FIN / 4 + 255) / 256, B256, 0, stream>>>(x, xb, NN * FIN / 4);
-    k_convB0<<<(512 * FIN + 255) / 256, B256, 0, stream>>>(W0, B0t);
-    k_convBm<<<(3 * HIDD * 512 + 255) / 256, B256, 0, stream>>>(Wm, Bmt);
-    k_convBL<<<(48 * HIDD + 255) / 256, B256, 0, stream>>>(WL, WLt);
+    k_tables<<<(10112 + 255) / 256, B256, 0, stream>>>(
+        rel0, relm, relL, aedge0, aedgem, aedgeL, Wm, asrcm, adstm, WL, asrcL, adstL,
+        etab, wsmb, wdmb, WLt, aS48, aD48);
+    k_casts<<<(BM_END + 255) / 256, B256, 0, stream>>>(x, W0, Wm, xb, B0t, Bmt);
 
     int mblk = (NN + 127) / 128;
 
     {
         dim3 g(mblk, 4);
-        k_mfma_gemm<<<g, 256, 0, stream>>>(xb, B0t, NN, FIN, 512, 1.f, h0b, nullptr,
-                                           nullptr, nullptr, asrc0, adst0, es, ed);
+        k_mfma_gemm<<<g, 256, 0, stream>>>(xb, B0t, NN, FIN, 512, h0b, asrc0, adst0, es, ed);
         k_agg0_f<<<NN, 64, 0, stream>>>(rowptr, srcp, etpp, distwp, es, ed, etab + 0,
                                         h0b, b0, xbuf);
-    }
-
+        k_bnstats_at<<<200, 128, 0, stream>>>(xbuf, sums);
+    }
+
+    int gmid = (NN + 63) / 64;
     for (int i = 0; i < 3; ++i) {
-        k_bnstats<<<200, 128, 0, stream>>>(xbuf, bnpart);
-        k_bnfinal<<<1, 128, 0, stream>>>(bnpart, bng + i * 128, bnb + i * 128, scale, shift);
-        k_bnaps<<<NN, 64, 0, stream>>>(xbuf, scale, shift, wsmb + i * 512, wdmb + i * 512,
-                                       hb, hbb, es, ed);
+        k_bnaps<<<NN, 64, 0, stream>>>(xbuf, sums + i * 256, bng + i * 128, bnb + i * 128,
+                                       wsmb + i * 512, wdmb + i * 512, hb, hbb, es, ed);
         k_aggmid_f<<<NN, 64, 0, stream>>>(rowptr, srcp, etpp, distwp, es, ed,
                                           etab + (1 + i) * 160, hbb, h0b);
-        dim3 g(mblk, 1);
-        k_mfma_gemm<<<g, 256, 0, stream>>>(h0b, Bmt + (size_t)i * HIDD * 512, NN, 512, HIDD,
-                                           0.25f, nullptr, xbuf, bm + i * 128, hb,
-                                           nullptr, nullptr, nullptr, nullptr);
+        k_gemm_mid<<<gmid, 128, 0, stream>>>(h0b, Bmt + (size_t)i * HIDD * 512, xbuf,
+                                             bm + i * 128, hb, sums + (i + 1) * 256);
     }
 
     {
-        k_bnstats<<<200, 128, 0, stream>>>(xbuf, bnpart);
-        k_bnfinal<<<1, 128, 0, stream>>>(bnpart, bng + 3 * 128, bnb + 3 * 128, scale, shift);
-        k_bnaps<<<NN, 64, 0, stream>>>(xbuf, scale, shift, nullptr, nullptr, hb, hbb, es, ed);
-        k_gemmL_mfma<<<(NN + 63) / 64, 256, 0, stream>>>(hbb, WLt, hL);
-        k_scoresL<<<gNN, B256, 0, stream>>>(hL, asrcL, adstL, es, ed);
+        k_bnaps<<<NN, 64, 0, stream>>>(xbuf, sums + 3 * 256, bng + 3 * 128, bnb + 3 * 128,
+                                       nullptr, nullptr, hb, hbb, es, ed);
+        k_gemmL_mfma<<<(NN + 63) / 64, 256, 0, stream>>>(hbb, WLt, hL, aS48, aD48, es, ed);
         k_aggL_f<<<NN, 64, 0, stream>>>(rowptr, srcp, etpp, distwp, es, ed, etab + 4 * 160,
                                         hL, bL, out);
     }
```

New measurement: 562.1 us. -15.2%, faster.
